# Optimization experiments

Hardware: AMD Instinct MI355X
Metric: run time of the kernel (lower is better)

The kernel has to match this reference:

```python
import jax, jax.numpy as jnp
import numpy as np

B, S, D = 2, 2048, 2048
H, DH = 16, 128  # heads, dhead


def setup_inputs() -> dict:
    key = jax.random.key(0)
    k1, k2, k3 = jax.random.split(key, 3)
    x = jax.random.normal(k1, (B, S, D), dtype=jnp.float32)
    # torch Linear weights: [out_features, in_features], fan_in-scaled init
    w_in = jax.random.normal(k2, (3 * H * DH, D), dtype=jnp.float32) * (1.0 / np.sqrt(D))
    w_out = jax.random.normal(k3, (D, H * DH), dtype=jnp.float32) * (1.0 / np.sqrt(H * DH))
    return {"x": x, "w_in": w_in, "w_out": w_out}


def reference(x, w_in, w_out):
    b, s, _ = x.shape
    # input projection (no bias): [b, s, 3*H*DH]
    projected = jnp.einsum("bsd,ed->bse", x, w_in)
    # view(b, s, H, 3*DH) then chunk along last dim -> q, k, v each [b, s, H, DH]
    projected = projected.reshape(b, s, H, 3 * DH)
    q, k, v = jnp.split(projected, 3, axis=-1)
    # naive path: scores [b, H, s, s]
    scores = jnp.einsum("bqhd,bkhd->bhqk", q, k) * (1.0 / np.sqrt(DH))
    # causal mask (tril keeps, upper triangle -> -inf)
    causal_mask = jnp.tril(jnp.ones((s, s), dtype=bool))
    scores = jnp.where(causal_mask, scores, jnp.float32(-jnp.inf))
    attn = jax.nn.softmax(scores, axis=-1)
    # PV: [b, s, H, DH]
    out = jnp.einsum("bhqk,bkhd->bqhd", attn, v)
    out = out.reshape(b, s, H * DH)
    # output projection (no bias): [b, s, D]
    return jnp.einsum("bse,de->bsd", out, w_out)
```

## Files before the change

### kernel.cpp

```cpp
#include <hip/hip_runtime.h>
#include <hip/hip_bf16.h>
#include <math.h>


typedef short bf16x8 __attribute__((ext_vector_type(8)));
typedef float f32x4 __attribute__((ext_vector_type(4)));

#define NEG_BIG -30000.0f

__device__ __forceinline__ short f2bf(float f) {
    union { float f; unsigned u; } v; v.f = f;
    unsigned r = v.u + 0x7fffu + ((v.u >> 16) & 1u);
    return (short)(r >> 16);
}

__device__ __forceinline__ int pack2bf(float a, float b) {
    return (int)((((unsigned)f2bf(b)) << 16) | (((unsigned)f2bf(a)) & 0xffffu));
}

#define GLDS16(g, l) \
    __builtin_amdgcn_global_load_lds((const __attribute__((address_space(1))) void*)(g), \
                                     (__attribute__((address_space(3))) void*)(l), 16, 0, 0)

__global__ __launch_bounds__(256) void cvt_f32_bf16(const float* __restrict__ src,
                                                    short* __restrict__ dst, int n) {
    int i = (blockIdx.x * blockDim.x + threadIdx.x) * 4;
    if (i < n) {
        float4 v = *(const float4*)(src + i);
        short4 o;
        o.x = f2bf(v.x); o.y = f2bf(v.y); o.z = f2bf(v.z); o.w = f2bf(v.w);
        *(short4*)(dst + i) = o;
    }
}

template <bool F32OUT>
__global__ __launch_bounds__(256) void gemm_bt(const short* __restrict__ A,
                                               const short* __restrict__ Bm,
                                               void* __restrict__ Cv,
                                               int N, int K) {
    __shared__ short sA[128 * 32];
    __shared__ short sB[128 * 32];
    const int lane = threadIdx.x & 63;
    const int w = threadIdx.x >> 6;
    const int l15 = lane & 15, quad = lane >> 4;
    const int bm0 = blockIdx.y * 128, bn0 = blockIdx.x * 128;

    const int c1 = w * 64 + lane;
    const short* gA = A + (size_t)(bm0 + (c1 >> 2)) * K + (c1 & 3) * 8;
    const short* gB = Bm + (size_t)(bn0 + (c1 >> 2)) * K + (c1 & 3) * 8;
    const size_t half = (size_t)64 * K;
    short* lA1 = sA + w * 512;
    short* lA2 = sA + 2048 + w * 512;
    short* lB1 = sB + w * 512;
    short* lB2 = sB + 2048 + w * 512;

    const int wm = (w >> 1) * 64, wn = (w & 1) * 64;
    const short* pa = sA + (wm + l15) * 32 + quad * 8;
    const short* pb = sB + (wn + l15) * 32 + quad * 8;

    f32x4 acc[4][4] = {};
    for (int k0 = 0; k0 < K; k0 += 32) {
        GLDS16(gA + k0, lA1);
        GLDS16(gA + half + k0, lA2);
        GLDS16(gB + k0, lB1);
        GLDS16(gB + half + k0, lB2);
        __syncthreads();
        bf16x8 af[4], bf[4];
        #pragma unroll
        for (int mt = 0; mt < 4; mt++) af[mt] = *(const bf16x8*)(pa + mt * 512);
        #pragma unroll
        for (int nt = 0; nt < 4; nt++) bf[nt] = *(const bf16x8*)(pb + nt * 512);
        #pragma unroll
        for (int mt = 0; mt < 4; mt++)
            #pragma unroll
            for (int nt = 0; nt < 4; nt++)
                acc[mt][nt] = __builtin_amdgcn_mfma_f32_16x16x32_bf16(af[mt], bf[nt], acc[mt][nt], 0, 0, 0);
        __syncthreads();
    }
    #pragma unroll
    for (int mt = 0; mt < 4; mt++)
        #pragma unroll
        for (int nt = 0; nt < 4; nt++)
            #pragma unroll
            for (int r = 0; r < 4; r++) {
                int row = bm0 + wm + mt * 16 + quad * 4 + r;
                int col = bn0 + wn + nt * 16 + l15;
                if (F32OUT)
                    ((float*)Cv)[(size_t)row * N + col] = acc[mt][nt][r];
                else
                    ((short*)Cv)[(size_t)row * N + col] = f2bf(acc[mt][nt][r]);
            }
}

#define VP 40
__global__ __launch_bounds__(256) void attn_kernel(const short* __restrict__ P,
                                                   short* __restrict__ O) {
    constexpr int S = 2048, ROWW = 6144, HD = 2048;
    const int id = blockIdx.x;
    const int b = id >> 9;
    const int rr = id & 511;
    const int h = rr & 15;
    const int t0 = rr >> 4;
    const int qt = (t0 < 16) ? t0 : 47 - t0;
    const int wave = threadIdx.x >> 6, lane = threadIdx.x & 63;
    const int l15 = lane & 15, quad = lane >> 4;
    const int qRow = qt * 64 + wave * 16;
    const short* Pb = P + (size_t)b * S * ROWW;
    const short* Qp = Pb + h * 384;
    const short* Kp = Qp + 128;
    const short* Vp = Qp + 256;

    __shared__ short sK[2][32 * 128];
    __shared__ short sVt[2][128 * VP];

    bf16x8 qf[4];
    #pragma unroll
    for (int f = 0; f < 4; f++)
        qf[f] = *(const bf16x8*)(Qp + (size_t)(qRow + l15) * ROWW + f * 32 + quad * 8);

    const int c1 = wave * 64 + lane;
    const int krow1 = c1 >> 4;
    const int kcol = (((c1 & 15) ^ (krow1 & 15)) * 8);
    const short* gK1 = Kp + (size_t)krow1 * ROWW + kcol;
    const short* gK2 = Kp + (size_t)(krow1 + 16) * ROWW + kcol;
    const int ldsOff1 = wave * 512;
    const int ldsOff2 = 2048 + wave * 512;

    const int tid = threadIdx.x;
    const int vKey = tid & 31;
    const int vD0 = (tid >> 5) * 8;
    const short* gV = Vp + (size_t)vKey * ROWW + vD0;

    const int kTiles = (qt * 2 + 2 < 64) ? (qt * 2 + 2) : 64;
    const float scale = 0.08838834764831845f;
    const int qG = qRow + l15;

    f32x4 accO[8] = {};
    float m_i = NEG_BIG, l_i = 0.f;

    GLDS16(gK1, &sK[0][ldsOff1]);
    GLDS16(gK2, &sK[0][ldsOff2]);
    {
        bf16x8 v0 = *(const bf16x8*)(gV);
        bf16x8 v1 = *(const bf16x8*)(gV + 64);
        #pragma unroll
        for (int j = 0; j < 8; j++) {
            sVt[0][(vD0 + j) * VP + vKey] = v0[j];
            sVt[0][(vD0 + 64 + j) * VP + vKey] = v1[j];
        }
    }
    __syncthreads();

    for (int kt = 0; kt < kTiles; kt++) {
        const int cur = kt & 1, nxt = cur ^ 1;
        const bool pre = (kt + 1 < kTiles);
        bf16x8 v0n, v1n;
        if (pre) {
            const size_t kOff = (size_t)(kt + 1) * 32 * ROWW;
            GLDS16(gK1 + kOff, &sK[nxt][ldsOff1]);
            GLDS16(gK2 + kOff, &sK[nxt][ldsOff2]);
            v0n = *(const bf16x8*)(gV + kOff);
            v1n = *(const bf16x8*)(gV + kOff + 64);
        }
        f32x4 sc[2] = {};
        #pragma unroll
        for (int hh = 0; hh < 2; hh++) {
            const int row = hh * 16 + l15;
            #pragma unroll
            for (int f = 0; f < 4; f++) {
                const int jj = (4 * f + quad) ^ l15;
                bf16x8 kf = *(const bf16x8*)(&sK[cur][row * 128 + jj * 8]);
                sc[hh] = __builtin_amdgcn_mfma_f32_16x16x32_bf16(kf, qf[f], sc[hh], 0, 0, 0);
            }
        }
        #pragma unroll
        for (int hh = 0; hh < 2; hh++)
            #pragma unroll
            for (int r = 0; r < 4; r++) {
                int key = kt * 32 + hh * 16 + quad * 4 + r;
                float v = sc[hh][r] * scale;
                sc[hh][r] = (key <= qG) ? v : NEG_BIG;
            }
        float mloc = sc[0][0];
        #pragma unroll
        for (int r = 1; r < 4; r++) mloc = fmaxf(mloc, sc[0][r]);
        #pragma unroll
        for (int r = 0; r < 4; r++) mloc = fmaxf(mloc, sc[1][r]);
        mloc = fmaxf(mloc, __shfl_xor(mloc, 16));
        mloc = fmaxf(mloc, __shfl_xor(mloc, 32));
        const float nm = fmaxf(m_i, mloc);
        const float alpha = __expf(m_i - nm);
        m_i = nm;
        float ssum = 0.f;
        #pragma unroll
        for (int hh = 0; hh < 2; hh++)
            #pragma unroll
            for (int r = 0; r < 4; r++) {
                float p = __expf(sc[hh][r] - nm);
                sc[hh][r] = p;
                ssum += p;
            }
        ssum += __shfl_xor(ssum, 16);
        ssum += __shfl_xor(ssum, 32);
        l_i = alpha * l_i + ssum;
        #pragma unroll
        for (int t = 0; t < 8; t++)
            #pragma unroll
            for (int r = 0; r < 4; r++) accO[t][r] *= alpha;
        const int d00 = pack2bf(sc[0][0], sc[0][1]);
        const int d01 = pack2bf(sc[0][2], sc[0][3]);
        const int d10 = pack2bf(sc[1][0], sc[1][1]);
        const int d11 = pack2bf(sc[1][2], sc[1][3]);
        const int srcA = l15 + ((quad & 1) << 5);
        const int srcB = srcA + 16;
        const int s00 = __shfl(d00, srcA), s01 = __shfl(d01, srcA);
        const int s02 = __shfl(d00, srcB), s03 = __shfl(d01, srcB);
        const int s10 = __shfl(d10, srcA), s11 = __shfl(d11, srcA);
        const int s12 = __shfl(d10, srcB), s13 = __shfl(d11, srcB);
        union { int i[4]; bf16x8 v; } pu;
        const bool lo = quad < 2;
        pu.i[0] = lo ? s00 : s10;
        pu.i[1] = lo ? s01 : s11;
        pu.i[2] = lo ? s02 : s12;
        pu.i[3] = lo ? s03 : s13;
        const bf16x8 pf = pu.v;
        #pragma unroll
        for (int t = 0; t < 8; t++) {
            bf16x8 vf = *(const bf16x8*)(&sVt[cur][(t * 16 + l15) * VP + quad * 8]);
            accO[t] = __builtin_amdgcn_mfma_f32_16x16x32_bf16(vf, pf, accO[t], 0, 0, 0);
        }
        if (pre) {
            #pragma unroll
            for (int j = 0; j < 8; j++) {
                sVt[nxt][(vD0 + j) * VP + vKey] = v0n[j];
                sVt[nxt][(vD0 + 64 + j) * VP + vKey] = v1n[j];
            }
        }
        __syncthreads();
    }
    const float inv = 1.0f / l_i;
    #pragma unroll
    for (int t = 0; t < 8; t++) {
        short4 st;
        st.x = f2bf(accO[t][0] * inv);
        st.y = f2bf(accO[t][1] * inv);
        st.z = f2bf(accO[t][2] * inv);
        st.w = f2bf(accO[t][3] * inv);
        *(short4*)(&O[(size_t)(b * S + qG) * HD + h * 128 + t * 16 + quad * 4]) = st;
    }
}

extern "C" void kernel_launch(void* const* d_in, const int* in_sizes, int n_in,
                              void* d_out, int out_size, void* d_ws, size_t ws_size,
                              hipStream_t stream) {
    const float* x     = (const float*)d_in[0];
    const float* w_in  = (const float*)d_in[1];
    const float* w_out = (const float*)d_in[2];
    float* out = (float*)d_out;

    short* Pbuf   = (short*)d_ws;
    short* xObuf  = Pbuf  + (size_t)4096 * 6144;
    short* winb   = xObuf + (size_t)8388608;
    short* woutb  = winb  + (size_t)6144 * 2048;

    dim3 blk(256, 1, 1);
    const int nx = 2 * 2048 * 2048, nwi = 6144 * 2048, nwo = 2048 * 2048;
    hipLaunchKernelGGL(cvt_f32_bf16, dim3(nx / 1024), blk, 0, stream, x, xObuf, nx);
    hipLaunchKernelGGL(cvt_f32_bf16, dim3(nwi / 1024), blk, 0, stream, w_in, winb, nwi);
    hipLaunchKernelGGL(cvt_f32_bf16, dim3(nwo / 1024), blk, 0, stream, w_out, woutb, nwo);
    hipLaunchKernelGGL((gemm_bt<false>), dim3(48, 32, 1), blk, 0, stream, xObuf, winb, (void*)Pbuf, 6144, 2048);
    hipLaunchKernelGGL(attn_kernel, dim3(1024, 1, 1), blk, 0, stream, Pbuf, xObuf);
    hipLaunchKernelGGL((gemm_bt<true>), dim3(16, 32, 1), blk, 0, stream, xObuf, woutb, (void*)out, 2048, 2048);
}
```

Before: 443.0 us.

## Use 128-row attention blocks with split K/V loader waves and narrower output GEMM tile

The attention kernel now runs 512-thread blocks covering 128 query rows, so each K/V tile loaded into shared memory is reused by eight waves instead of four. Waves 0-3 load K and waves 4-7 load and transpose V, where before every thread loaded both. Causal load balancing now pairs the two batches in reverse tile order instead of folding tiles within a batch. The output projection GEMM takes a BN template parameter and uses a 64-wide N tile, doubling its block count to fill more CUs, at the cost of less reuse of the A tile.

```diff
diff --git a/kernel.cpp b/kernel.cpp
--- a/kernel.cpp
+++ b/kernel.cpp
@@ -33,54 +33,55 @@
     }
 }
 
-template <bool F32OUT>
+template <int BN, bool F32OUT>
 __global__ __launch_bounds__(256) void gemm_bt(const short* __restrict__ A,
                                                const short* __restrict__ Bm,
                                                void* __restrict__ Cv,
                                                int N, int K) {
+    constexpr int NT = BN / 32;
     __shared__ short sA[128 * 32];
-    __shared__ short sB[128 * 32];
+    __shared__ short sB[BN * 32];
     const int lane = threadIdx.x & 63;
     const int w = threadIdx.x >> 6;
     const int l15 = lane & 15, quad = lane >> 4;
-    const int bm0 = blockIdx.y * 128, bn0 = blockIdx.x * 128;
+    const int bm0 = blockIdx.y * 128, bn0 = blockIdx.x * BN;
 
     const int c1 = w * 64 + lane;
     const short* gA = A + (size_t)(bm0 + (c1 >> 2)) * K + (c1 & 3) * 8;
     const short* gB = Bm + (size_t)(bn0 + (c1 >> 2)) * K + (c1 & 3) * 8;
-    const size_t half = (size_t)64 * K;
+    const size_t halfA = (size_t)64 * K;
     short* lA1 = sA + w * 512;
     short* lA2 = sA + 2048 + w * 512;
     short* lB1 = sB + w * 512;
     short* lB2 = sB + 2048 + w * 512;
 
-    const int wm = (w >> 1) * 64, wn = (w & 1) * 64;
+    const int wm = (w >> 1) * 64, wn = (w & 1) * (BN / 2);
     const short* pa = sA + (wm + l15) * 32 + quad * 8;
     const short* pb = sB + (wn + l15) * 32 + quad * 8;
 
-    f32x4 acc[4][4] = {};
+    f32x4 acc[4][NT] = {};
     for (int k0 = 0; k0 < K; k0 += 32) {
         GLDS16(gA + k0, lA1);
-        GLDS16(gA + half + k0, lA2);
+        GLDS16(gA + halfA + k0, lA2);
         GLDS16(gB + k0, lB1);
-        GLDS16(gB + half + k0, lB2);
+        if constexpr (BN == 128) GLDS16(gB + halfA + k0, lB2);
         __syncthreads();
-        bf16x8 af[4], bf[4];
+        bf16x8 af[4], bf[NT];
         #pragma unroll
         for (int mt = 0; mt < 4; mt++) af[mt] = *(const bf16x8*)(pa + mt * 512);
         #pragma unroll
-        for (int nt = 0; nt < 4; nt++) bf[nt] = *(const bf16x8*)(pb + nt * 512);
+        for (int nt = 0; nt < NT; nt++) bf[nt] = *(const bf16x8*)(pb + nt * 512);
         #pragma unroll
         for (int mt = 0; mt < 4; mt++)
             #pragma unroll
-            for (int nt = 0; nt < 4; nt++)
+            for (int nt = 0; nt < NT; nt++)
                 acc[mt][nt] = __builtin_amdgcn_mfma_f32_16x16x32_bf16(af[mt], bf[nt], acc[mt][nt], 0, 0, 0);
         __syncthreads();
     }
     #pragma unroll
     for (int mt = 0; mt < 4; mt++)
         #pragma unroll
-        for (int nt = 0; nt < 4; nt++)
+        for (int nt = 0; nt < NT; nt++)
             #pragma unroll
             for (int r = 0; r < 4; r++) {
                 int row = bm0 + wm + mt * 16 + quad * 4 + r;
@@ -93,18 +94,18 @@
 }
 
 #define VP 40
-__global__ __launch_bounds__(256) void attn_kernel(const short* __restrict__ P,
+__global__ __launch_bounds__(512) void attn_kernel(const short* __restrict__ P,
                                                    short* __restrict__ O) {
     constexpr int S = 2048, ROWW = 6144, HD = 2048;
     const int id = blockIdx.x;
-    const int b = id >> 9;
-    const int rr = id & 511;
+    const int b = id >> 8;
+    const int rr = id & 255;
     const int h = rr & 15;
     const int t0 = rr >> 4;
-    const int qt = (t0 < 16) ? t0 : 47 - t0;
+    const int qt = b ? (15 - t0) : t0;
     const int wave = threadIdx.x >> 6, lane = threadIdx.x & 63;
     const int l15 = lane & 15, quad = lane >> 4;
-    const int qRow = qt * 64 + wave * 16;
+    const int qRow = qt * 128 + wave * 16;
     const short* Pb = P + (size_t)b * S * ROWW;
     const short* Qp = Pb + h * 384;
     const short* Kp = Qp + 128;
@@ -118,29 +119,30 @@
     for (int f = 0; f < 4; f++)
         qf[f] = *(const bf16x8*)(Qp + (size_t)(qRow + l15) * ROWW + f * 32 + quad * 8);
 
-    const int c1 = wave * 64 + lane;
+    const bool isK = wave < 4;
+    const int c1 = (wave & 3) * 64 + lane;
     const int krow1 = c1 >> 4;
-    const int kcol = (((c1 & 15) ^ (krow1 & 15)) * 8);
+    const int kcol = ((c1 & 15) ^ (krow1 & 15)) * 8;
     const short* gK1 = Kp + (size_t)krow1 * ROWW + kcol;
     const short* gK2 = Kp + (size_t)(krow1 + 16) * ROWW + kcol;
-    const int ldsOff1 = wave * 512;
-    const int ldsOff2 = 2048 + wave * 512;
-
-    const int tid = threadIdx.x;
-    const int vKey = tid & 31;
-    const int vD0 = (tid >> 5) * 8;
+    const int ldsOff1 = (wave & 3) * 512;
+    const int ldsOff2 = 2048 + (wave & 3) * 512;
+    const int vt = (int)threadIdx.x - 256;
+    const int vKey = vt & 31;
+    const int vD0 = (vt >> 5) * 8;
     const short* gV = Vp + (size_t)vKey * ROWW + vD0;
 
-    const int kTiles = (qt * 2 + 2 < 64) ? (qt * 2 + 2) : 64;
+    const int kTiles = qt * 4 + 4;
     const float scale = 0.08838834764831845f;
     const int qG = qRow + l15;
 
     f32x4 accO[8] = {};
     float m_i = NEG_BIG, l_i = 0.f;
 
-    GLDS16(gK1, &sK[0][ldsOff1]);
-    GLDS16(gK2, &sK[0][ldsOff2]);
-    {
+    if (isK) {
+        GLDS16(gK1, &sK[0][ldsOff1]);
+        GLDS16(gK2, &sK[0][ldsOff2]);
+    } else {
         bf16x8 v0 = *(const bf16x8*)(gV);
         bf16x8 v1 = *(const bf16x8*)(gV + 64);
         #pragma unroll
@@ -157,10 +159,13 @@
         bf16x8 v0n, v1n;
         if (pre) {
             const size_t kOff = (size_t)(kt + 1) * 32 * ROWW;
-            GLDS16(gK1 + kOff, &sK[nxt][ldsOff1]);
-            GLDS16(gK2 + kOff, &sK[nxt][ldsOff2]);
-            v0n = *(const bf16x8*)(gV + kOff);
-            v1n = *(const bf16x8*)(gV + kOff + 64);
+            if (isK) {
+                GLDS16(gK1 + kOff, &sK[nxt][ldsOff1]);
+                GLDS16(gK2 + kOff, &sK[nxt][ldsOff2]);
+            } else {
+                v0n = *(const bf16x8*)(gV + kOff);
+                v1n = *(const bf16x8*)(gV + kOff + 64);
+            }
         }
         f32x4 sc[2] = {};
         #pragma unroll
@@ -229,7 +234,7 @@
             bf16x8 vf = *(const bf16x8*)(&sVt[cur][(t * 16 + l15) * VP + quad * 8]);
             accO[t] = __builtin_amdgcn_mfma_f32_16x16x32_bf16(vf, pf, accO[t], 0, 0, 0);
         }
-        if (pre) {
+        if (pre && !isK) {
             #pragma unroll
             for (int j = 0; j < 8; j++) {
                 sVt[nxt][(vD0 + j) * VP + vKey] = v0n[j];
@@ -268,7 +273,7 @@
     hipLaunchKernelGGL(cvt_f32_bf16, dim3(nx / 1024), blk, 0, stream, x, xObuf, nx);
     hipLaunchKernelGGL(cvt_f32_bf16, dim3(nwi / 1024), blk, 0, stream, w_in, winb, nwi);
     hipLaunchKernelGGL(cvt_f32_bf16, dim3(nwo / 1024), blk, 0, stream, w_out, woutb, nwo);
-    hipLaunchKernelGGL((gemm_bt<false>), dim3(48, 32, 1), blk, 0, stream, xObuf, winb, (void*)Pbuf, 6144, 2048);
-    hipLaunchKernelGGL(attn_kernel, dim3(1024, 1, 1), blk, 0, stream, Pbuf, xObuf);
-    hipLaunchKernelGGL((gemm_bt<true>), dim3(16, 32, 1), blk, 0, stream, xObuf, woutb, (void*)out, 2048, 2048);
-}
+    hipLaunchKernelGGL((gemm_bt<128, false>), dim3(48, 32, 1), blk, 0, stream, xObuf, winb, (void*)Pbuf, 6144, 2048);
+    hipLaunchKernelGGL(attn_kernel, dim3(512, 1, 1), dim3(512, 1, 1), 0, stream, Pbuf, xObuf);
+    hipLaunchKernelGGL((gemm_bt<64, true>), dim3(32, 32, 1), blk, 0, stream, xObuf, woutb, (void*)out, 2048, 2048);
+}
```

Result: faster. 414.1 us (-6.5%).
